# Performance work log

Hardware: AMD Instinct MI355X
Metric: run time of the kernel (lower is better)

## Reference

```python
import jax, jax.numpy as jnp
import numpy as np

B, L, E, Q = 32, 2048, 512, 512

def setup_inputs() -> dict:
    key = jax.random.key(0)
    k1, k2, k3, k4, k5 = jax.random.split(key, 5)
    scale_attn = 1.0 / np.sqrt(E + Q)
    scale_v = 1.0 / np.sqrt(E)
    return {
        "embeddings": jax.random.normal(k1, (B, L, E), dtype=jnp.float32),
        "query": jax.random.normal(k2, (B, L, Q), dtype=jnp.float32),
        "W_attn": jax.random.normal(k3, (E, E + Q), dtype=jnp.float32) * scale_attn,
        "b_attn": jax.random.normal(k4, (E,), dtype=jnp.float32) * scale_attn,
        "v_w": jax.random.normal(k5, (E,), dtype=jnp.float32) * scale_v,
    }

def reference(embeddings, query, W_attn, b_attn, v_w):
    # concat along feature dim: (B, L, Q+E)
    cat = jnp.concatenate([query, embeddings], axis=2)
    # attn_layer: Linear(E+Q -> E), then tanh: (B, L, E)
    h = jnp.tanh(jnp.einsum('blf,ef->ble', cat, W_attn) + b_attn)
    # attn_v: Linear(E -> 1, no bias) -> scores (B, L)
    scores = jnp.einsum('ble,e->bl', h, v_w)
    # softmax over the sequence (dim=1 in torch)
    w = jax.nn.softmax(scores, axis=1)  # (B, L)
    # transpose to (B, 1, L) then bmm with embeddings -> (B, 1, E)
    applied = jnp.einsum('bl,ble->be', w, embeddings)[:, None, :]
    weights = w[:, None, :]
    return (applied, weights)
```

## Files before the change

### kernel.cpp

```cpp
#include <hip/hip_runtime.h>
#include <hip/hip_bf16.h>
#include <math.h>


typedef __attribute__((ext_vector_type(8))) short bf16x8;
typedef __attribute__((ext_vector_type(4))) float f32x4;

#define BDIM 32
#define LDIM 2048
#define EDIM 512
#define QDIM 512
#define KDIM 1024
#define MDIM (BDIM * LDIM)

#define BM 128
#define BN 128
#define BK 64
#define NSTEPS (KDIM / BK)

__device__ __forceinline__ unsigned int pack2bf(float lo, float hi) {
    unsigned int a = __builtin_bit_cast(unsigned int, lo) + 0x8000u;
    unsigned int b = __builtin_bit_cast(unsigned int, hi) + 0x8000u;
    return __builtin_amdgcn_perm(b, a, 0x07060302);
}

__global__ __launch_bounds__(256) void convert_w_kernel(
    const float* __restrict__ W, unsigned short* __restrict__ Wsw)
{
    const int gid = blockIdx.x * 256 + threadIdx.x;
    const int n  = gid >> 7;
    const int jb = (gid & 127) * 16;
    const int sb = jb ^ ((n & 7) << 4);
    const float* src = W + (size_t)n * KDIM + (sb >> 2);
    src = W + (size_t)n * KDIM + (sb >> 1);
    const float4 a = *(const float4*)(src);
    const float4 c = *(const float4*)(src + 4);
    uint4 o;
    o.x = pack2bf(a.x, a.y); o.y = pack2bf(a.z, a.w);
    o.z = pack2bf(c.x, c.y); o.w = pack2bf(c.z, c.w);
    *(uint4*)((char*)Wsw + (size_t)n * 2048 + jb) = o;
}

__device__ __forceinline__ bf16x8 lds_frag(const unsigned short* buf, int row, int cb) {
    return *(const bf16x8*)((const char*)buf + row * 128 + (cb ^ ((row & 7) << 4)));
}

__device__ __forceinline__ void load_a(const float* __restrict__ emb,
                                       const float* __restrict__ query,
                                       int m0, int kstep, int arow, int acol,
                                       float4 (&r)[8])
{
    const int k0 = kstep * BK;
    const float* asrc = (k0 < QDIM) ? query : emb;
    const int koff = (k0 < QDIM) ? k0 : (k0 - QDIM);
    #pragma unroll
    for (int p = 0; p < 8; p++)
        r[p] = *(const float4*)(asrc + (size_t)(m0 + p * 16 + arow) * 512 + koff + acol);
}

__device__ __forceinline__ void write_a(unsigned short* buf, int arow, int acolb,
                                        int axor, const float4 (&r)[8])
{
    #pragma unroll
    for (int p = 0; p < 8; p++) {
        uint2 pk;
        pk.x = pack2bf(r[p].x, r[p].y);
        pk.y = pack2bf(r[p].z, r[p].w);
        *(uint2*)((char*)buf + (p * 16 + arow) * 128 + (acolb ^ axor)) = pk;
    }
}

__device__ __forceinline__ void gll_b(const unsigned short* __restrict__ Wsw,
                                      unsigned short* buf, int n0, int kstep,
                                      int brow, int bcb, int wvoff)
{
    const size_t kb = (size_t)kstep * (BK * 2);
    #pragma unroll
    for (int p = 0; p < 4; p++) {
        const char* g = (const char*)Wsw + (size_t)(n0 + p * 32 + brow) * 2048 + kb + bcb;
        __builtin_amdgcn_global_load_lds(
            (const __attribute__((address_space(1))) void*)g,
            (__attribute__((address_space(3))) void*)((char*)buf + p * 4096 + wvoff),
            16, 0, 0);
    }
}

__device__ __forceinline__ void compute_step(const unsigned short* a_,
                                             const unsigned short* b_,
                                             int wm, int wn, int ln, int quad,
                                             f32x4 (&acc)[4][4])
{
    __builtin_amdgcn_s_setprio(1);
    #pragma unroll
    for (int ks = 0; ks < 2; ks++) {
        bf16x8 af[4], bf_[4];
        #pragma unroll
        for (int i = 0; i < 4; i++) af[i] = lds_frag(a_, wm + i * 16 + ln, ks * 64 + quad * 16);
        #pragma unroll
        for (int j = 0; j < 4; j++) bf_[j] = lds_frag(b_, wn + j * 16 + ln, ks * 64 + quad * 16);
        #pragma unroll
        for (int i = 0; i < 4; i++)
            #pragma unroll
            for (int j = 0; j < 4; j++)
                acc[i][j] = __builtin_amdgcn_mfma_f32_16x16x32_bf16(af[i], bf_[j], acc[i][j], 0, 0, 0);
    }
    __builtin_amdgcn_s_setprio(0);
}

__global__ __launch_bounds__(256, 2) void scores_kernel(
    const float* __restrict__ emb, const float* __restrict__ query,
    const unsigned short* __restrict__ Wsw, const float* __restrict__ b_attn,
    const float* __restrict__ v_w, float* __restrict__ scores)
{
    __shared__ __align__(16) unsigned short As[2][BM * BK];
    __shared__ __align__(16) unsigned short Bs[2][BN * BK];

    const int tid = threadIdx.x;
    const int bid = blockIdx.x;
    const int xcd = bid & 7;
    const int slot = bid >> 3;
    const int mtile = xcd * 64 + (slot >> 2);
    const int ntile = slot & 3;
    const int m0 = mtile * BM;
    const int n0 = ntile * BN;

    const int lane = tid & 63;
    const int wv = tid >> 6;
    const int wm = (wv >> 1) * 64;
    const int wn = (wv & 1) * 64;
    const int quad = lane >> 4;
    const int ln = lane & 15;

    const int arow  = tid >> 4;
    const int acol  = (tid & 15) * 4;
    const int acolb = acol * 2;
    const int axor  = (arow & 7) << 4;

    const int brow = tid >> 3;
    const int bcb  = (tid & 7) * 16;
    const int wvoff = __builtin_amdgcn_readfirstlane((tid >> 6) << 10);

    f32x4 acc[4][4];
    #pragma unroll
    for (int i = 0; i < 4; i++)
        #pragma unroll
        for (int j = 0; j < 4; j++)
            acc[i][j] = (f32x4){0.f, 0.f, 0.f, 0.f};

    float4 ra[8], rb[8];

    load_a(emb, query, m0, 0, arow, acol, ra);
    write_a(&As[0][0], arow, acolb, axor, ra);
    gll_b(Wsw, &Bs[0][0], n0, 0, brow, bcb, wvoff);
    load_a(emb, query, m0, 1, arow, acol, rb);
    __syncthreads();

    for (int t = 0; t < NSTEPS; t += 2) {
        if (t < NSTEPS - 2) load_a(emb, query, m0, t + 2, arow, acol, ra);
        write_a(&As[1][0], arow, acolb, axor, rb);
        gll_b(Wsw, &Bs[1][0], n0, t + 1, brow, bcb, wvoff);
        compute_step(&As[0][0], &Bs[0][0], wm, wn, ln, quad, acc);
        __syncthreads();

        if (t + 1 < NSTEPS - 1) {
            if (t + 1 < NSTEPS - 2) load_a(emb, query, m0, t + 3, arow, acol, rb);
            write_a(&As[0][0], arow, acolb, axor, ra);
            gll_b(Wsw, &Bs[0][0], n0, t + 2, brow, bcb, wvoff);
        }
        compute_step(&As[1][0], &Bs[1][0], wm, wn, ln, quad, acc);
        __syncthreads();
    }

    float bj[4], vj[4];
    #pragma unroll
    for (int j = 0; j < 4; j++) {
        const int n = n0 + wn + j * 16 + ln;
        bj[j] = b_attn[n];
        vj[j] = v_w[n];
    }
    #pragma unroll
    for (int i = 0; i < 4; i++) {
        #pragma unroll
        for (int r = 0; r < 4; r++) {
            float s = 0.f;
            #pragma unroll
            for (int j = 0; j < 4; j++)
                s += tanhf(acc[i][j][r] + bj[j]) * vj[j];
            #pragma unroll
            for (int off = 1; off < 16; off <<= 1)
                s += __shfl_xor(s, off, 64);
            if (ln == 0)
                atomicAdd(&scores[m0 + wm + i * 16 + quad * 4 + r], s);
        }
    }
}

__global__ __launch_bounds__(256) void softmax_apply_kernel(
    const float* __restrict__ emb, const float* __restrict__ scores,
    float* __restrict__ out_applied, float* __restrict__ out_weights)
{
    const int b = blockIdx.x >> 6;
    const int chunk = blockIdx.x & 63;
    const int l0 = chunk * 32;
    const int tid = threadIdx.x;
    const float* srow = scores + (size_t)b * LDIM;

    __shared__ float red[4];
    __shared__ float wls[32];
    __shared__ float partial[512];

    float sv[8];
    #pragma unroll
    for (int t = 0; t < 8; t++) sv[t] = srow[tid + t * 256];

    float mx = sv[0];
    #pragma unroll
    for (int t = 1; t < 8; t++) mx = fmaxf(mx, sv[t]);
    #pragma unroll
    for (int off = 1; off < 64; off <<= 1) mx = fmaxf(mx, __shfl_xor(mx, off, 64));
    if ((tid & 63) == 0) red[tid >> 6] = mx;
    __syncthreads();
    mx = fmaxf(fmaxf(red[0], red[1]), fmaxf(red[2], red[3]));

    float sm = 0.f;
    #pragma unroll
    for (int t = 0; t < 8; t++) sm += expf(sv[t] - mx);
    #pragma unroll
    for (int off = 1; off < 64; off <<= 1) sm += __shfl_xor(sm, off, 64);
    __syncthreads();
    if ((tid & 63) == 0) red[tid >> 6] = sm;
    __syncthreads();
    sm = red[0] + red[1] + red[2] + red[3];
    const float inv = 1.f / sm;

    if (tid < 32) {
        const float w = expf(srow[l0 + tid] - mx) * inv;
        wls[tid] = w;
        out_weights[(size_t)b * LDIM + l0 + tid] = w;
    }
    __syncthreads();

    const int half = tid >> 7;
    const int cg = tid & 127;
    float4 acc = {0.f, 0.f, 0.f, 0.f};
    const float* ebase = emb + ((size_t)b * LDIM + l0 + half) * EDIM + cg * 4;
    #pragma unroll
    for (int i = 0; i < 16; i++) {
        const float4 v = *(const float4*)(ebase + (size_t)2 * i * EDIM);
        const float w = wls[half + 2 * i];
        acc.x += w * v.x;
        acc.y += w * v.y;
        acc.z += w * v.z;
        acc.w += w * v.w;
    }
    if (half == 1) *(float4*)&partial[cg * 4] = acc;
    __syncthreads();
    if (half == 0) {
        const float4 p = *(const float4*)&partial[cg * 4];
        float* dst = out_applied + (size_t)b * EDIM + cg * 4;
        atomicAdd(dst + 0, acc.x + p.x);
        atomicAdd(dst + 1, acc.y + p.y);
        atomicAdd(dst + 2, acc.z + p.z);
        atomicAdd(dst + 3, acc.w + p.w);
    }
}

extern "C" void kernel_launch(void* const* d_in, const int* in_sizes, int n_in,
                              void* d_out, int out_size, void* d_ws, size_t ws_size,
                              hipStream_t stream) {
    const float* emb    = (const float*)d_in[0];
    const float* query  = (const float*)d_in[1];
    const float* W      = (const float*)d_in[2];
    const float* b_attn = (const float*)d_in[3];
    const float* v_w    = (const float*)d_in[4];

    float* out     = (float*)d_out;
    float* applied = out;
    float* weights = out + BDIM * EDIM;

    float* scores  = (float*)d_ws;
    unsigned short* Wsw = (unsigned short*)((char*)d_ws + (size_t)MDIM * 4);

    hipMemsetAsync(scores, 0, (size_t)MDIM * sizeof(float), stream);
    hipMemsetAsync(applied, 0, (size_t)BDIM * EDIM * sizeof(float), stream);

    convert_w_kernel<<<256, 256, 0, stream>>>(W, Wsw);

    scores_kernel<<<2048, 256, 0, stream>>>(emb, query, Wsw, b_attn, v_w, scores);

    softmax_apply_kernel<<<2048, 256, 0, stream>>>(emb, scores, applied, weights);
}
```

Measured before the change: 387.2 us.

## Halve GEMM K-tile for higher occupancy and split softmax from weighted sum

The scores GEMM now uses a K-tile of 32 instead of 64. That halves LDS and register use per block and raises the launch bound to 4 blocks per CU, with the weight swizzle and LDS layouts redone to match. The softmax stage is split into a per-batch stats kernel that writes the weights once, followed by an apply kernel over 64-row chunks. This removes the repeated full-row softmax recomputation that the old kernel did in every block. The cost is twice as many K iterations and barriers in the GEMM, plus an extra kernel launch.

```diff
diff --git a/kernel.cpp b/kernel.cpp
--- a/kernel.cpp
+++ b/kernel.cpp
@@ -15,7 +15,7 @@
 
 #define BM 128
 #define BN 128
-#define BK 64
+#define BK 32
 #define NSTEPS (KDIM / BK)
 
 __device__ __forceinline__ unsigned int pack2bf(float lo, float hi) {
@@ -28,86 +28,80 @@
     const float* __restrict__ W, unsigned short* __restrict__ Wsw)
 {
     const int gid = blockIdx.x * 256 + threadIdx.x;
-    const int n  = gid >> 7;
-    const int jb = (gid & 127) * 16;
-    const int sb = jb ^ ((n & 7) << 4);
-    const float* src = W + (size_t)n * KDIM + (sb >> 2);
-    src = W + (size_t)n * KDIM + (sb >> 1);
+    const int n   = gid >> 7;
+    const int rem = gid & 127;
+    const int g   = rem >> 2;
+    const int t   = rem & 3;
+    const int srcslot = t ^ ((n >> 1) & 3);
+    const float* src = W + (size_t)n * KDIM + g * 32 + srcslot * 8;
     const float4 a = *(const float4*)(src);
     const float4 c = *(const float4*)(src + 4);
     uint4 o;
     o.x = pack2bf(a.x, a.y); o.y = pack2bf(a.z, a.w);
     o.z = pack2bf(c.x, c.y); o.w = pack2bf(c.z, c.w);
-    *(uint4*)((char*)Wsw + (size_t)n * 2048 + jb) = o;
-}
-
-__device__ __forceinline__ bf16x8 lds_frag(const unsigned short* buf, int row, int cb) {
-    return *(const bf16x8*)((const char*)buf + row * 128 + (cb ^ ((row & 7) << 4)));
+    *(uint4*)((char*)Wsw + (size_t)n * 2048 + g * 64 + t * 16) = o;
 }
 
 __device__ __forceinline__ void load_a(const float* __restrict__ emb,
                                        const float* __restrict__ query,
                                        int m0, int kstep, int arow, int acol,
-                                       float4 (&r)[8])
+                                       float4 (&r)[4])
 {
     const int k0 = kstep * BK;
     const float* asrc = (k0 < QDIM) ? query : emb;
     const int koff = (k0 < QDIM) ? k0 : (k0 - QDIM);
     #pragma unroll
-    for (int p = 0; p < 8; p++)
-        r[p] = *(const float4*)(asrc + (size_t)(m0 + p * 16 + arow) * 512 + koff + acol);
+    for (int p = 0; p < 4; p++)
+        r[p] = *(const float4*)(asrc + (size_t)(m0 + p * 32 + arow) * 512 + koff + acol);
 }
 
 __device__ __forceinline__ void write_a(unsigned short* buf, int arow, int acolb,
-                                        int axor, const float4 (&r)[8])
-{
-    #pragma unroll
-    for (int p = 0; p < 8; p++) {
+                                        int axor, const float4 (&r)[4])
+{
+    #pragma unroll
+    for (int p = 0; p < 4; p++) {
         uint2 pk;
         pk.x = pack2bf(r[p].x, r[p].y);
         pk.y = pack2bf(r[p].z, r[p].w);
-        *(uint2*)((char*)buf + (p * 16 + arow) * 128 + (acolb ^ axor)) = pk;
+        *(uint2*)((char*)buf + (p * 32 + arow) * 64 + (acolb ^ axor)) = pk;
     }
 }
 
 __device__ __forceinline__ void gll_b(const unsigned short* __restrict__ Wsw,
                                       unsigned short* buf, int n0, int kstep,
-                                      int brow, int bcb, int wvoff)
-{
-    const size_t kb = (size_t)kstep * (BK * 2);
-    #pragma unroll
-    for (int p = 0; p < 4; p++) {
-        const char* g = (const char*)Wsw + (size_t)(n0 + p * 32 + brow) * 2048 + kb + bcb;
+                                      int brow0, int bslot, int wvoff)
+{
+    const size_t kb = (size_t)kstep * 64;
+    #pragma unroll
+    for (int q = 0; q < 2; q++) {
+        const char* g = (const char*)Wsw + (size_t)(n0 + q * 64 + brow0) * 2048 + kb + bslot * 16;
         __builtin_amdgcn_global_load_lds(
             (const __attribute__((address_space(1))) void*)g,
-            (__attribute__((address_space(3))) void*)((char*)buf + p * 4096 + wvoff),
+            (__attribute__((address_space(3))) void*)((char*)buf + q * 4096 + wvoff),
             16, 0, 0);
     }
 }
 
 __device__ __forceinline__ void compute_step(const unsigned short* a_,
                                              const unsigned short* b_,
-                                             int wm, int wn, int ln, int quad,
+                                             int abase, int bbase,
                                              f32x4 (&acc)[4][4])
 {
     __builtin_amdgcn_s_setprio(1);
-    #pragma unroll
-    for (int ks = 0; ks < 2; ks++) {
-        bf16x8 af[4], bf_[4];
+    bf16x8 af[4], bfr[4];
+    #pragma unroll
+    for (int i = 0; i < 4; i++) af[i] = *(const bf16x8*)((const char*)a_ + abase + i * 1024);
+    #pragma unroll
+    for (int j = 0; j < 4; j++) bfr[j] = *(const bf16x8*)((const char*)b_ + bbase + j * 1024);
+    #pragma unroll
+    for (int i = 0; i < 4; i++)
         #pragma unroll
-        for (int i = 0; i < 4; i++) af[i] = lds_frag(a_, wm + i * 16 + ln, ks * 64 + quad * 16);
-        #pragma unroll
-        for (int j = 0; j < 4; j++) bf_[j] = lds_frag(b_, wn + j * 16 + ln, ks * 64 + quad * 16);
-        #pragma unroll
-        for (int i = 0; i < 4; i++)
-            #pragma unroll
-            for (int j = 0; j < 4; j++)
-                acc[i][j] = __builtin_amdgcn_mfma_f32_16x16x32_bf16(af[i], bf_[j], acc[i][j], 0, 0, 0);
-    }
+        for (int j = 0; j < 4; j++)
+            acc[i][j] = __builtin_amdgcn_mfma_f32_16x16x32_bf16(af[i], bfr[j], acc[i][j], 0, 0, 0);
     __builtin_amdgcn_s_setprio(0);
 }
 
-__global__ __launch_bounds__(256, 2) void scores_kernel(
+__global__ __launch_bounds__(256, 4) void scores_kernel(
     const float* __restrict__ emb, const float* __restrict__ query,
     const unsigned short* __restrict__ Wsw, const float* __restrict__ b_attn,
     const float* __restrict__ v_w, float* __restrict__ scores)
@@ -131,14 +125,18 @@
     const int quad = lane >> 4;
     const int ln = lane & 15;
 
-    const int arow  = tid >> 4;
-    const int acol  = (tid & 15) * 4;
+    const int arow  = tid >> 3;
+    const int acol  = (tid & 7) * 4;
     const int acolb = acol * 2;
-    const int axor  = (arow & 7) << 4;
-
-    const int brow = tid >> 3;
-    const int bcb  = (tid & 7) * 16;
-    const int wvoff = __builtin_amdgcn_readfirstlane((tid >> 6) << 10);
+    const int axor  = ((arow >> 1) & 3) << 4;
+
+    const int brow0 = wv * 16 + (lane >> 2);
+    const int bslot = lane & 3;
+    const int wvoff = __builtin_amdgcn_readfirstlane(wv << 10);
+
+    const int fxor  = ((ln >> 1) & 3) << 4;
+    const int abase = (wm + ln) * 64 + ((quad * 16) ^ fxor);
+    const int bbase = (wn + ln) * 64 + ((quad * 16) ^ fxor);
 
     f32x4 acc[4][4];
     #pragma unroll
@@ -147,27 +145,27 @@
         for (int j = 0; j < 4; j++)
             acc[i][j] = (f32x4){0.f, 0.f, 0.f, 0.f};
 
-    float4 ra[8], rb[8];
+    float4 ra[4], rb[4];
 
     load_a(emb, query, m0, 0, arow, acol, ra);
     write_a(&As[0][0], arow, acolb, axor, ra);
-    gll_b(Wsw, &Bs[0][0], n0, 0, brow, bcb, wvoff);
+    gll_b(Wsw, &Bs[0][0], n0, 0, brow0, bslot, wvoff);
     load_a(emb, query, m0, 1, arow, acol, rb);
     __syncthreads();
 
     for (int t = 0; t < NSTEPS; t += 2) {
         if (t < NSTEPS - 2) load_a(emb, query, m0, t + 2, arow, acol, ra);
         write_a(&As[1][0], arow, acolb, axor, rb);
-        gll_b(Wsw, &Bs[1][0], n0, t + 1, brow, bcb, wvoff);
-        compute_step(&As[0][0], &Bs[0][0], wm, wn, ln, quad, acc);
+        gll_b(Wsw, &Bs[1][0], n0, t + 1, brow0, bslot, wvoff);
+        compute_step(&As[0][0], &Bs[0][0], abase, bbase, acc);
         __syncthreads();
 
         if (t + 1 < NSTEPS - 1) {
             if (t + 1 < NSTEPS - 2) load_a(emb, query, m0, t + 3, arow, acol, rb);
             write_a(&As[0][0], arow, acolb, axor, ra);
-            gll_b(Wsw, &Bs[0][0], n0, t + 2, brow, bcb, wvoff);
+            gll_b(Wsw, &Bs[0][0], n0, t + 2, brow0, bslot, wvoff);
         }
-        compute_step(&As[1][0], &Bs[1][0], wm, wn, ln, quad, acc);
+        compute_step(&As[1][0], &Bs[1][0], abase, bbase, acc);
         __syncthreads();
     }
 
@@ -195,19 +193,13 @@
     }
 }
 
-__global__ __launch_bounds__(256) void softmax_apply_kernel(
-    const float* __restrict__ emb, const float* __restrict__ scores,
-    float* __restrict__ out_applied, float* __restrict__ out_weights)
-{
-    const int b = blockIdx.x >> 6;
-    const int chunk = blockIdx.x & 63;
-    const int l0 = chunk * 32;
+__global__ __launch_bounds__(256) void softmax_stats_kernel(
+    const float* __restrict__ scores, float* __restrict__ out_weights)
+{
+    const int b = blockIdx.x;
     const int tid = threadIdx.x;
     const float* srow = scores + (size_t)b * LDIM;
-
     __shared__ float red[4];
-    __shared__ float wls[32];
-    __shared__ float partial[512];
 
     float sv[8];
     #pragma unroll
@@ -233,25 +225,38 @@
     sm = red[0] + red[1] + red[2] + red[3];
     const float inv = 1.f / sm;
 
-    if (tid < 32) {
-        const float w = expf(srow[l0 + tid] - mx) * inv;
-        wls[tid] = w;
-        out_weights[(size_t)b * LDIM + l0 + tid] = w;
-    }
+    #pragma unroll
+    for (int t = 0; t < 8; t++)
+        out_weights[(size_t)b * LDIM + tid + t * 256] = expf(sv[t] - mx) * inv;
+}
+
+__global__ __launch_bounds__(256) void apply_kernel(
+    const float* __restrict__ emb, const float* __restrict__ w,
+    float* __restrict__ out_applied)
+{
+    const int b = blockIdx.x >> 5;
+    const int chunk = blockIdx.x & 31;
+    const int l0 = chunk * 64;
+    const int tid = threadIdx.x;
+
+    __shared__ float wls[64];
+    __shared__ float partial[512];
+
+    if (tid < 64) wls[tid] = w[(size_t)b * LDIM + l0 + tid];
     __syncthreads();
 
     const int half = tid >> 7;
     const int cg = tid & 127;
     float4 acc = {0.f, 0.f, 0.f, 0.f};
     const float* ebase = emb + ((size_t)b * LDIM + l0 + half) * EDIM + cg * 4;
-    #pragma unroll
-    for (int i = 0; i < 16; i++) {
+    #pragma unroll 8
+    for (int i = 0; i < 32; i++) {
         const float4 v = *(const float4*)(ebase + (size_t)2 * i * EDIM);
-        const float w = wls[half + 2 * i];
-        acc.x += w * v.x;
-        acc.y += w * v.y;
-        acc.z += w * v.z;
-        acc.w += w * v.w;
+        const float ww = wls[half + 2 * i];
+        acc.x += ww * v.x;
+        acc.y += ww * v.y;
+        acc.z += ww * v.z;
+        acc.w += ww * v.w;
     }
     if (half == 1) *(float4*)&partial[cg * 4] = acc;
     __syncthreads();
@@ -288,5 +293,7 @@
 
     scores_kernel<<<2048, 256, 0, stream>>>(emb, query, Wsw, b_attn, v_w, scores);
 
-    softmax_apply_kernel<<<2048, 256, 0, stream>>>(emb, scores, applied, weights);
-}
+    softmax_stats_kernel<<<32, 256, 0, stream>>>(scores, weights);
+
+    apply_kernel<<<1024, 256, 0, stream>>>(emb, weights, applied);
+}
```

Result: slower. 438.4 us (+13.2%).

## Relax loop barriers, replace score atomics with partials, split softmax stats

Applied to the files above, without the earlier changes.

The GEMM main loop now uses a custom barrier that waits only until vmcnt(8), so prefetched global loads can stay in flight across the sync. The loads are also reordered so the B DMA is issued before the A loads. Score accumulation writes per-N-tile partials after an in-LDS reduction instead of global atomics, which removes the scores memset. Softmax statistics are computed once per batch row in a separate small kernel rather than being recomputed by every apply block. The relaxed waitcnt risks reading LDS data that has not arrived yet, and the split adds one more kernel launch.

```diff
diff --git a/kernel.cpp b/kernel.cpp
--- a/kernel.cpp
+++ b/kernel.cpp
@@ -18,6 +18,12 @@
 #define BK 64
 #define NSTEPS (KDIM / BK)
 
+#define BAR() do { \
+    asm volatile("s_waitcnt vmcnt(8) lgkmcnt(0)" ::: "memory"); \
+    __builtin_amdgcn_s_barrier(); \
+    __builtin_amdgcn_sched_barrier(0); \
+} while (0)
+
 __device__ __forceinline__ unsigned int pack2bf(float lo, float hi) {
     unsigned int a = __builtin_bit_cast(unsigned int, lo) + 0x8000u;
     unsigned int b = __builtin_bit_cast(unsigned int, hi) + 0x8000u;
@@ -31,8 +37,7 @@
     const int n  = gid >> 7;
     const int jb = (gid & 127) * 16;
     const int sb = jb ^ ((n & 7) << 4);
-    const float* src = W + (size_t)n * KDIM + (sb >> 2);
-    src = W + (size_t)n * KDIM + (sb >> 1);
+    const float* src = W + (size_t)n * KDIM + (sb >> 1);
     const float4 a = *(const float4*)(src);
     const float4 c = *(const float4*)(src + 4);
     uint4 o;
@@ -93,16 +98,16 @@
     __builtin_amdgcn_s_setprio(1);
     #pragma unroll
     for (int ks = 0; ks < 2; ks++) {
-        bf16x8 af[4], bf_[4];
+        bf16x8 af[4], bfr[4];
         #pragma unroll
         for (int i = 0; i < 4; i++) af[i] = lds_frag(a_, wm + i * 16 + ln, ks * 64 + quad * 16);
         #pragma unroll
-        for (int j = 0; j < 4; j++) bf_[j] = lds_frag(b_, wn + j * 16 + ln, ks * 64 + quad * 16);
+        for (int j = 0; j < 4; j++) bfr[j] = lds_frag(b_, wn + j * 16 + ln, ks * 64 + quad * 16);
         #pragma unroll
         for (int i = 0; i < 4; i++)
             #pragma unroll
             for (int j = 0; j < 4; j++)
-                acc[i][j] = __builtin_amdgcn_mfma_f32_16x16x32_bf16(af[i], bf_[j], acc[i][j], 0, 0, 0);
+                acc[i][j] = __builtin_amdgcn_mfma_f32_16x16x32_bf16(af[i], bfr[j], acc[i][j], 0, 0, 0);
     }
     __builtin_amdgcn_s_setprio(0);
 }
@@ -110,7 +115,7 @@
 __global__ __launch_bounds__(256, 2) void scores_kernel(
     const float* __restrict__ emb, const float* __restrict__ query,
     const unsigned short* __restrict__ Wsw, const float* __restrict__ b_attn,
-    const float* __restrict__ v_w, float* __restrict__ scores)
+    const float* __restrict__ v_w, float* __restrict__ part)
 {
     __shared__ __align__(16) unsigned short As[2][BM * BK];
     __shared__ __align__(16) unsigned short Bs[2][BN * BK];
@@ -150,25 +155,30 @@
     float4 ra[8], rb[8];
 
     load_a(emb, query, m0, 0, arow, acol, ra);
-    write_a(&As[0][0], arow, acolb, axor, ra);
     gll_b(Wsw, &Bs[0][0], n0, 0, brow, bcb, wvoff);
     load_a(emb, query, m0, 1, arow, acol, rb);
-    __syncthreads();
+    write_a(&As[0][0], arow, acolb, axor, ra);
+    BAR();
 
     for (int t = 0; t < NSTEPS; t += 2) {
-        if (t < NSTEPS - 2) load_a(emb, query, m0, t + 2, arow, acol, ra);
+        gll_b(Wsw, &Bs[1][0], n0, t + 1, brow, bcb, wvoff);
+        {
+            const int kpre = (t + 2 < NSTEPS) ? t + 2 : NSTEPS - 1;
+            load_a(emb, query, m0, kpre, arow, acol, ra);
+        }
         write_a(&As[1][0], arow, acolb, axor, rb);
-        gll_b(Wsw, &Bs[1][0], n0, t + 1, brow, bcb, wvoff);
         compute_step(&As[0][0], &Bs[0][0], wm, wn, ln, quad, acc);
-        __syncthreads();
-
-        if (t + 1 < NSTEPS - 1) {
-            if (t + 1 < NSTEPS - 2) load_a(emb, query, m0, t + 3, arow, acol, rb);
+        BAR();
+
+        {
+            const int kst = (t + 2 < NSTEPS) ? t + 2 : NSTEPS - 1;
+            gll_b(Wsw, &Bs[0][0], n0, kst, brow, bcb, wvoff);
+            const int kpre = (t + 3 < NSTEPS) ? t + 3 : NSTEPS - 1;
+            load_a(emb, query, m0, kpre, arow, acol, rb);
             write_a(&As[0][0], arow, acolb, axor, ra);
-            gll_b(Wsw, &Bs[0][0], n0, t + 2, brow, bcb, wvoff);
         }
         compute_step(&As[1][0], &Bs[1][0], wm, wn, ln, quad, acc);
-        __syncthreads();
+        BAR();
     }
 
     float bj[4], vj[4];
@@ -178,6 +188,8 @@
         bj[j] = b_attn[n];
         vj[j] = v_w[n];
     }
+    float* redbuf = (float*)&As[0][0];
+    const int half = wn >> 6;
     #pragma unroll
     for (int i = 0; i < 4; i++) {
         #pragma unroll
@@ -190,54 +202,69 @@
             for (int off = 1; off < 16; off <<= 1)
                 s += __shfl_xor(s, off, 64);
             if (ln == 0)
-                atomicAdd(&scores[m0 + wm + i * 16 + quad * 4 + r], s);
+                redbuf[half * 128 + wm + i * 16 + quad * 4 + r] = s;
         }
     }
-}
-
-__global__ __launch_bounds__(256) void softmax_apply_kernel(
-    const float* __restrict__ emb, const float* __restrict__ scores,
-    float* __restrict__ out_applied, float* __restrict__ out_weights)
+    __syncthreads();
+    if (tid < 128)
+        part[(size_t)ntile * MDIM + m0 + tid] = redbuf[tid] + redbuf[128 + tid];
+}
+
+__global__ __launch_bounds__(256) void softmax_stats_kernel(
+    const float* __restrict__ part, float* __restrict__ out_weights)
+{
+    const int b = blockIdx.x;
+    const int tid = threadIdx.x;
+    __shared__ float red[4];
+
+    float sv[8];
+    #pragma unroll
+    for (int t = 0; t < 8; t++) {
+        const size_t idx = (size_t)b * LDIM + tid + t * 256;
+        float s = part[idx];
+        #pragma unroll
+        for (int j = 1; j < 4; j++) s += part[(size_t)j * MDIM + idx];
+        sv[t] = s;
+    }
+
+    float mx = sv[0];
+    #pragma unroll
+    for (int t = 1; t < 8; t++) mx = fmaxf(mx, sv[t]);
+    #pragma unroll
+    for (int off = 1; off < 64; off <<= 1) mx = fmaxf(mx, __shfl_xor(mx, off, 64));
+    if ((tid & 63) == 0) red[tid >> 6] = mx;
+    __syncthreads();
+    mx = fmaxf(fmaxf(red[0], red[1]), fmaxf(red[2], red[3]));
+
+    float sm = 0.f;
+    #pragma unroll
+    for (int t = 0; t < 8; t++) sm += expf(sv[t] - mx);
+    #pragma unroll
+    for (int off = 1; off < 64; off <<= 1) sm += __shfl_xor(sm, off, 64);
+    __syncthreads();
+    if ((tid & 63) == 0) red[tid >> 6] = sm;
+    __syncthreads();
+    sm = red[0] + red[1] + red[2] + red[3];
+    const float inv = 1.f / sm;
+
+    #pragma unroll
+    for (int t = 0; t < 8; t++)
+        out_weights[(size_t)b * LDIM + tid + t * 256] = expf(sv[t] - mx) * inv;
+}
+
+__global__ __launch_bounds__(256) void apply_kernel(
+    const float* __restrict__ emb, const float* __restrict__ w,
+    float* __restrict__ out_applied)
 {
     const int b = blockIdx.x >> 6;
     const int chunk = blockIdx.x & 63;
     const int l0 = chunk * 32;
     const int tid = threadIdx.x;
-    const float* srow = scores + (size_t)b * LDIM;
-
-    __shared__ float red[4];
+
     __shared__ float wls[32];
     __shared__ float partial[512];
 
-    float sv[8];
-    #pragma unroll
-    for (int t = 0; t < 8; t++) sv[t] = srow[tid + t * 256];
-
-    float mx = sv[0];
-    #pragma unroll
-    for (int t = 1; t < 8; t++) mx = fmaxf(mx, sv[t]);
-    #pragma unroll
-    for (int off = 1; off < 64; off <<= 1) mx = fmaxf(mx, __shfl_xor(mx, off, 64));
-    if ((tid & 63) == 0) red[tid >> 6] = mx;
-    __syncthreads();
-    mx = fmaxf(fmaxf(red[0], red[1]), fmaxf(red[2], red[3]));
-
-    float sm = 0.f;
-    #pragma unroll
-    for (int t = 0; t < 8; t++) sm += expf(sv[t] - mx);
-    #pragma unroll
-    for (int off = 1; off < 64; off <<= 1) sm += __shfl_xor(sm, off, 64);
-    __syncthreads();
-    if ((tid & 63) == 0) red[tid >> 6] = sm;
-    __syncthreads();
-    sm = red[0] + red[1] + red[2] + red[3];
-    const float inv = 1.f / sm;
-
-    if (tid < 32) {
-        const float w = expf(srow[l0 + tid] - mx) * inv;
-        wls[tid] = w;
-        out_weights[(size_t)b * LDIM + l0 + tid] = w;
-    }
+    if (tid < 32) wls[tid] = w[(size_t)b * LDIM + l0 + tid];
     __syncthreads();
 
     const int half = tid >> 7;
@@ -247,11 +274,11 @@
     #pragma unroll
     for (int i = 0; i < 16; i++) {
         const float4 v = *(const float4*)(ebase + (size_t)2 * i * EDIM);
-        const float w = wls[half + 2 * i];
-        acc.x += w * v.x;
-        acc.y += w * v.y;
-        acc.z += w * v.z;
-        acc.w += w * v.w;
+        const float ww = wls[half + 2 * i];
+        acc.x += ww * v.x;
+        acc.y += ww * v.y;
+        acc.z += ww * v.z;
+        acc.w += ww * v.w;
     }
     if (half == 1) *(float4*)&partial[cg * 4] = acc;
     __syncthreads();
@@ -278,15 +305,16 @@
     float* applied = out;
     float* weights = out + BDIM * EDIM;
 
-    float* scores  = (float*)d_ws;
-    unsigned short* Wsw = (unsigned short*)((char*)d_ws + (size_t)MDIM * 4);
-
-    hipMemsetAsync(scores, 0, (size_t)MDIM * sizeof(float), stream);
+    float* part = (float*)d_ws;
+    unsigned short* Wsw = (unsigned short*)((char*)d_ws + (size_t)4 * MDIM * 4);
+
     hipMemsetAsync(applied, 0, (size_t)BDIM * EDIM * sizeof(float), stream);
 
     convert_w_kernel<<<256, 256, 0, stream>>>(W, Wsw);
 
-    scores_kernel<<<2048, 256, 0, stream>>>(emb, query, Wsw, b_attn, v_w, scores);
-
-    softmax_apply_kernel<<<2048, 256, 0, stream>>>(emb, scores, applied, weights);
-}
+    scores_kernel<<<2048, 256, 0, stream>>>(emb, query, Wsw, b_attn, v_w, part);
+
+    softmax_stats_kernel<<<32, 256, 0, stream>>>(part, weights);
+
+    apply_kernel<<<2048, 256, 0, stream>>>(emb, weights, applied);
+}
```

Result: no change. 392.1 us (+1.3%).
